# Kernel optimization log

Hardware: AMD Instinct MI355X
Metric: run time of the kernel (lower is better)

## Reference

```python
import jax, jax.numpy as jnp
import numpy as np

B, S, H = 2, 2048, 2048
NH, NKV, HD = 16, 4, 128
THETA = 10000.0


def _rope_cos_sin(seq_len, head_dim, theta, dtype):
    inv_freq = 1.0 / (theta ** (jnp.arange(0, head_dim, 2, dtype=jnp.float32) / head_dim))
    t = jnp.arange(seq_len, dtype=jnp.float32)
    freqs = t[:, None] * inv_freq[None, :]          # [S, HD/2]
    emb = jnp.concatenate([freqs, freqs], axis=-1)  # [S, HD]
    return jnp.cos(emb).astype(dtype), jnp.sin(emb).astype(dtype)


def _rotate_half(x):
    d = x.shape[-1] // 2
    return jnp.concatenate([-x[..., d:], x[..., :d]], axis=-1)


def setup_inputs() -> dict:
    key = jax.random.key(0)
    ks = jax.random.split(key, 5)
    x = jax.random.normal(ks[0], (B, S, H), dtype=jnp.float32)
    Wq = jax.random.normal(ks[1], (NH * HD, H), dtype=jnp.float32) * 0.02
    Wk = jax.random.normal(ks[2], (NKV * HD, H), dtype=jnp.float32) * 0.02
    Wv = jax.random.normal(ks[3], (NKV * HD, H), dtype=jnp.float32) * 0.02
    Wo = jax.random.normal(ks[4], (H, H), dtype=jnp.float32) * 0.02
    causal = jnp.tril(jnp.ones((S, S), dtype=bool))
    attention_mask = jnp.where(causal, 0.0, -1e9).astype(jnp.float32)[None, None]  # [1,1,S,S]
    return {"x": x, "attention_mask": attention_mask, "Wq": Wq, "Wk": Wk, "Wv": Wv, "Wo": Wo}


def reference(x, attention_mask, Wq, Wk, Wv, Wo):
    b, s, _ = x.shape
    q = (x @ Wq.T).reshape(b, s, NH, HD).transpose(0, 2, 1, 3)    # [b,nh,s,hd]
    k = (x @ Wk.T).reshape(b, s, NKV, HD).transpose(0, 2, 1, 3)   # [b,nkv,s,hd]
    v = (x @ Wv.T).reshape(b, s, NKV, HD).transpose(0, 2, 1, 3)
    cos, sin = _rope_cos_sin(s, HD, THETA, x.dtype)               # [s,hd] each
    cos = cos[None, None]; sin = sin[None, None]
    q = q * cos + _rotate_half(q) * sin
    k = k * cos + _rotate_half(k) * sin
    rep = NH // NKV
    k = jnp.repeat(k, rep, axis=1)                                 # [b,nh,s,hd]
    v = jnp.repeat(v, rep, axis=1)
    scores = jnp.einsum('bhqd,bhkd->bhqk', q, k) / jnp.sqrt(jnp.asarray(HD, x.dtype))
    scores = scores + attention_mask
    attn = jax.nn.softmax(scores, axis=-1)
    out = jnp.einsum('bhqk,bhkd->bhqd', attn, v)                   # [b,nh,s,hd]
    out = out.transpose(0, 2, 1, 3).reshape(b, s, NH * HD)
    return out @ Wo.T
```

## Files before the change

kernel.cpp:

```cpp
#include <hip/hip_runtime.h>

typedef unsigned short u16;
typedef __bf16 bf16x8 __attribute__((ext_vector_type(8)));
typedef float f32x4 __attribute__((ext_vector_type(4)));
typedef short s16x4 __attribute__((ext_vector_type(4)));

#define S_LEN  2048
#define NHEADS 16
#define NKVH   4
#define HDIM   128
#define BB     2
#define MROWS  4096
#define QKV_N  3072
#define HID    2048

__device__ __forceinline__ u16 f2b(float f) {
  union { float f; unsigned u; } x; x.f = f;
  unsigned r = x.u + 0x7fffu + ((x.u >> 16) & 1u);
  return (u16)(r >> 16);
}
__device__ __forceinline__ float b2f(u16 v) {
  union { unsigned u; float f; } x; x.u = ((unsigned)v) << 16;
  return x.f;
}
__device__ __forceinline__ void gload_lds16(const u16* g, u16* l) {
  __builtin_amdgcn_global_load_lds((__attribute__((address_space(1))) void*)g,
                                   (__attribute__((address_space(3))) void*)l,
                                   16, 0, 0);
}
__device__ __forceinline__ unsigned cvtpk(float lo, float hi) {
  unsigned r;
  asm("v_cvt_pk_bf16_f32 %0, %1, %2" : "=v"(r) : "v"(lo), "v"(hi));
  return r;
}
__device__ __forceinline__ float fexp2(float x) {
  float r;
  asm("v_exp_f32 %0, %1" : "=v"(r) : "v"(x));
  return r;
}
#if __has_builtin(__builtin_amdgcn_mfma_f32_16x16x16bf16_1k)
__device__ __forceinline__ f32x4 mfma16(s16x4 a, s16x4 b, f32x4 c) {
  return __builtin_amdgcn_mfma_f32_16x16x16bf16_1k(a, b, c, 0, 0, 0);
}
#else
__device__ __forceinline__ f32x4 mfma16(s16x4 a, s16x4 b, f32x4 c) {
  f32x4 d;
  asm volatile("v_mfma_f32_16x16x16_bf16 %0, %1, %2, %3"
               : "=v"(d) : "v"(a), "v"(b), "v"(c));
  return d;
}
#endif

#define SBAR() do { __builtin_amdgcn_sched_barrier(0); \
                    __builtin_amdgcn_s_barrier();      \
                    __builtin_amdgcn_sched_barrier(0); } while (0)

#define PB_X   8192
#define PB_WQ  (PB_X + 4096)
#define PB_WK  (PB_WQ + 1024)
#define PB_WV  (PB_WK + 1024)
#define PB_WO  (PB_WV + 4096)
#define PB_CS  (PB_WO + 512)
__global__ void k_prep(const float* __restrict__ x,
                       const float* __restrict__ Wq, const float* __restrict__ Wk,
                       const float* __restrict__ Wv, const float* __restrict__ Wo,
                       u16* __restrict__ xb, u16* __restrict__ Wqkvb,
                       u16* __restrict__ Wob, float* __restrict__ cs)
{
  const int bid = blockIdx.x, tid = threadIdx.x;
  const float* src; u16* dst; int i;
  if (bid < PB_X)       { i = bid * 256 + tid;            src = x;  dst = xb; }
  else if (bid < PB_WQ) { i = (bid - PB_X) * 256 + tid;   src = Wq; dst = Wqkvb; }
  else if (bid < PB_WK) { i = (bid - PB_WQ) * 256 + tid;  src = Wk; dst = Wqkvb + (size_t)2048 * HID; }
  else if (bid < PB_WV) { i = (bid - PB_WK) * 256 + tid;  src = Wv; dst = Wqkvb + (size_t)2560 * HID; }
  else if (bid < PB_WO) { i = (bid - PB_WV) * 256 + tid;  src = Wo; dst = Wob; }
  else {
    const int p = (bid - PB_WO) * 256 + tid;
    const int s = p >> 6, j = p & 63;
    float inv = expf(-(float)j * 0.14391156831212787f);
    float ang = (float)s * inv;
    float c, sn; sincosf(ang, &sn, &c);
    cs[p * 2 + 0] = c; cs[p * 2 + 1] = sn;
    return;
  }
  float4 v = ((const float4*)src)[i];
  ushort4 o;
  o.x = f2b(v.x); o.y = f2b(v.y); o.z = f2b(v.z); o.w = f2b(v.w);
  ((ushort4*)dst)[i] = o;
}

#define MFMA_GRP(AV, BV, MO, NO)                                              \
  __builtin_amdgcn_s_setprio(1);                                              \
  _Pragma("unroll") for (int kk = 0; kk < 2; ++kk)                            \
  _Pragma("unroll") for (int mm = 0; mm < 4; ++mm)                            \
  _Pragma("unroll") for (int nn = 0; nn < 2; ++nn)                            \
    acc[(MO) + mm][(NO) + nn] = __builtin_amdgcn_mfma_f32_16x16x32_bf16(      \
        AV[kk][mm], BV[kk][nn], acc[(MO) + mm][(NO) + nn], 0, 0, 0);          \
  __builtin_amdgcn_s_setprio(0);

template <int OUT_BF16>
__global__ __launch_bounds__(512, 2) void k_gemm256(
    const u16* __restrict__ A, const u16* __restrict__ Bm, void* __restrict__ Cv,
    int M, int N, int K)
{
  __shared__ u16 AL[2][2][8192];
  __shared__ u16 BL[2][2][8192];
  const int tid = threadIdx.x;
  const int wave = tid >> 6, lane = tid & 63;
  const int l15 = lane & 15, l4 = lane >> 4;
  const int wr = wave >> 2, wc = wave & 3;
  const int gx = gridDim.x;
  const int nwg = gx * gridDim.y;
  int bid = blockIdx.y * gx + blockIdx.x;
  bid = (bid & 7) * (nwg >> 3) + (bid >> 3);
  const int col0 = (bid % gx) * 256, row0 = (bid / gx) * 256;

  int srcOff[2], dstD[2];
#pragma unroll
  for (int li = 0; li < 2; ++li) {
    const int D = (li * 512 + tid) * 16;
    const int off_p = D & 1023, si = D >> 10;
    const int off_l = off_p ^ (((off_p >> 9) & 1) << 5);
    const int R = si >> 1, C = si & 1;
    const int row = R * 16 + (off_l >> 6);
    const int colb = C * 64 + (off_l & 63);
    srcOff[li] = row * K + (colb >> 1);
    dstD[li] = D;
  }
  const int laneoff = (l15 * 64 + l4 * 16) ^ ((l15 >> 3) << 5);

  auto stage = [&](const u16* __restrict__ G, int grow0, int kb, u16* lds) {
#pragma unroll
    for (int li = 0; li < 2; ++li)
      gload_lds16(G + (size_t)grow0 * K + kb + srcOff[li],
                  (u16*)((char*)lds + dstD[li]));
  };

  f32x4 acc[8][4];
#pragma unroll
  for (int m = 0; m < 8; ++m)
#pragma unroll
    for (int n = 0; n < 4; ++n) acc[m][n] = f32x4{0.f, 0.f, 0.f, 0.f};

  const int nk = K >> 6;
  stage(A,  row0,       0,  &AL[0][0][0]);
  stage(A,  row0 + 128, 0,  &AL[0][1][0]);
  stage(Bm, col0,       0,  &BL[0][0][0]);
  stage(Bm, col0 + 128, 0,  &BL[0][1][0]);
  stage(A,  row0,       64, &AL[1][0][0]);
  stage(A,  row0 + 128, 64, &AL[1][1][0]);
  asm volatile("s_waitcnt vmcnt(4)" ::: "memory");
  SBAR();

  for (int t = 0; t < nk; ++t) {
    const int bi = t & 1;
    const bool sB = (t + 1 < nk);
    const bool sA = (t + 2 < nk);
    const char* Ab = (const char*)&AL[bi][wr][0];
    const char* Bb = (const char*)&BL[bi][wc >> 1][0] + (wc & 1) * 8192;
    bf16x8 a0[2][4], a1[2][4], b0[2][2], b1[2][2];
#pragma unroll
    for (int kk = 0; kk < 2; ++kk)
#pragma unroll
      for (int m = 0; m < 4; ++m)
        a0[kk][m] = *(const bf16x8*)(Ab + m * 2048 + kk * 1024 + laneoff);
#pragma unroll
    for (int kk = 0; kk < 2; ++kk)
#pragma unroll
      for (int n = 0; n < 2; ++n)
        b0[kk][n] = *(const bf16x8*)(Bb + n * 2048 + kk * 1024 + laneoff);
    if (sB) stage(Bm, col0, (t + 1) * 64, &BL[bi ^ 1][0][0]);
    SBAR();
    MFMA_GRP(a0, b0, 0, 0);
    SBAR();
#pragma unroll
    for (int kk = 0; kk < 2; ++kk)
#pragma unroll
      for (int m = 0; m < 4; ++m)
        a1[kk][m] = *(const bf16x8*)(Ab + (m + 4) * 2048 + kk * 1024 + laneoff);
    if (sB) stage(Bm, col0 + 128, (t + 1) * 64, &BL[bi ^ 1][1][0]);
    SBAR();
    MFMA_GRP(a1, b0, 4, 0);
    SBAR();
#pragma unroll
    for (int kk = 0; kk < 2; ++kk)
#pragma unroll
      for (int n = 0; n < 2; ++n)
        b1[kk][n] = *(const bf16x8*)(Bb + (n + 2) * 2048 + kk * 1024 + laneoff);
    if (sA) stage(A, row0, (t + 2) * 64, &AL[bi][0][0]);
    SBAR();
    MFMA_GRP(a1, b1, 4, 2);
    SBAR();
    if (sA) {
      stage(A, row0 + 128, (t + 2) * 64, &AL[bi][1][0]);
      asm volatile("s_waitcnt vmcnt(4)" ::: "memory");
    } else if (sB) {
      asm volatile("s_waitcnt vmcnt(0)" ::: "memory");
    }
    SBAR();
    MFMA_GRP(a0, b1, 0, 2);
    SBAR();
  }

#pragma unroll
  for (int m = 0; m < 8; ++m) {
    const int r = row0 + wr * 128 + m * 16 + l4 * 4;
#pragma unroll
    for (int n = 0; n < 4; ++n) {
      const int c = col0 + wc * 64 + n * 16 + l15;
#pragma unroll
      for (int j = 0; j < 4; ++j) {
        const float v = acc[m][n][j];
        if (OUT_BF16) ((u16*)Cv)[(size_t)(r + j) * N + c] = f2b(v);
        else          ((float*)Cv)[(size_t)(r + j) * N + c] = v;
      }
    }
  }
}

template <int OUT_BF16>
__global__ __launch_bounds__(256) void k_gemm_bt(
    const u16* __restrict__ A, const u16* __restrict__ Bm, void* __restrict__ Cv,
    int M, int N, int K)
{
  __shared__ u16 Al[128 * 32];
  __shared__ u16 Bl[128 * 32];
  const int tid = threadIdx.x;
  const int wave = tid >> 6, lane = tid & 63;
  const int l15 = lane & 15, l4 = lane >> 4;
  const int wr = wave >> 1, wc = wave & 1;
  const int row0 = blockIdx.y * 128, col0 = blockIdx.x * 128;

  f32x4 zero = {0.f, 0.f, 0.f, 0.f};
  f32x4 acc[4][4];
#pragma unroll
  for (int m = 0; m < 4; ++m)
#pragma unroll
    for (int n = 0; n < 4; ++n) acc[m][n] = zero;

  const int e0 = lane * 8;
  for (int kb = 0; kb < K; kb += 32) {
#pragma unroll
    for (int it = 0; it < 2; ++it) {
      const int chunk = it * 4 + wave;
      const int e = chunk * 512 + e0;
      const int r = e >> 5, c = e & 31;
      gload_lds16(A + (size_t)(row0 + r) * K + kb + c, Al + chunk * 512);
      gload_lds16(Bm + (size_t)(col0 + r) * K + kb + c, Bl + chunk * 512);
    }
    __syncthreads();
    bf16x8 af[4], bfv[4];
#pragma unroll
    for (int m = 0; m < 4; ++m)
      af[m] = *(const bf16x8*)(Al + (wr * 64 + m * 16 + l15) * 32 + l4 * 8);
#pragma unroll
    for (int n = 0; n < 4; ++n)
      bfv[n] = *(const bf16x8*)(Bl + (wc * 64 + n * 16 + l15) * 32 + l4 * 8);
#pragma unroll
    for (int m = 0; m < 4; ++m)
#pragma unroll
      for (int n = 0; n < 4; ++n)
        acc[m][n] = __builtin_amdgcn_mfma_f32_16x16x32_bf16(af[m], bfv[n], acc[m][n], 0, 0, 0);
    __syncthreads();
  }
#pragma unroll
  for (int m = 0; m < 4; ++m) {
    const int r = row0 + wr * 64 + m * 16 + l4 * 4;
#pragma unroll
    for (int n = 0; n < 4; ++n) {
      const int c = col0 + wc * 64 + n * 16 + l15;
#pragma unroll
      for (int j = 0; j < 4; ++j) {
        const float v = acc[m][n][j];
        if (OUT_BF16) ((u16*)Cv)[(size_t)(r + j) * N + c] = f2b(v);
        else          ((float*)Cv)[(size_t)(r + j) * N + c] = v;
      }
    }
  }
}

__global__ __launch_bounds__(256) void k_ropev(
    const u16* __restrict__ qkv, const float* __restrict__ cs,
    u16* __restrict__ Qr, u16* __restrict__ Kr, u16* __restrict__ Vt)
{
  const int blk = blockIdx.x;
  const int b = blk >> 8, s0 = (blk & 255) << 3;
  const int tid = threadIdx.x;
  const float S2 = 0.08838834764831845f * 1.4426950408889634f;
#pragma unroll
  for (int p = tid; p < 8192; p += 256) {
    const int s = p >> 10, rem = p & 1023, h = rem >> 6, j = rem & 63;
    const int sg = s0 + s;
    const float c = cs[(sg * 64 + j) * 2], sn = cs[(sg * 64 + j) * 2 + 1];
    const u16* src = qkv + (size_t)(b * S_LEN + sg) * QKV_N + h * 128;
    const float x0 = b2f(src[j]), x1 = b2f(src[64 + j]);
    const size_t base = ((size_t)(b * NHEADS + h) * S_LEN + sg) * HDIM;
    Qr[base + j]      = f2b((x0 * c - x1 * sn) * S2);
    Qr[base + 64 + j] = f2b((x1 * c + x0 * sn) * S2);
  }
#pragma unroll
  for (int p = tid; p < 2048; p += 256) {
    const int s = p >> 8, rem = p & 255, h = rem >> 6, j = rem & 63;
    const int sg = s0 + s;
    const float c = cs[(sg * 64 + j) * 2], sn = cs[(sg * 64 + j) * 2 + 1];
    const u16* src = qkv + (size_t)(b * S_LEN + sg) * QKV_N + 2048 + h * 128;
    const float x0 = b2f(src[j]), x1 = b2f(src[64 + j]);
    const size_t base = ((size_t)(b * NKVH + h) * S_LEN + sg) * HDIM;
    Kr[base + j]      = f2b(x0 * c - x1 * sn);
    Kr[base + 64 + j] = f2b(x1 * c + x0 * sn);
  }
#pragma unroll
  for (int vi = 0; vi < 2; ++vi) {
    const int idx = vi * 256 + tid, h = idx >> 7, d = idx & 127;
    union { u16 u[8]; uint4 v; } bb;
#pragma unroll
    for (int s = 0; s < 8; ++s)
      bb.u[s] = qkv[(size_t)(b * S_LEN + s0 + s) * QKV_N + 2560 + idx];
    *(uint4*)(Vt + ((size_t)(b * NKVH + h) * HDIM + d) * S_LEN + s0) = bb.v;
  }
}

__global__ __launch_bounds__(256) void k_attn(
    const u16* __restrict__ Q, const u16* __restrict__ Kr,
    const u16* __restrict__ Vt, u16* __restrict__ Out)
{
  __shared__ u16 Kl[2][64 * 128];
  __shared__ u16 Vl[2][128 * 64];
  const int tid = threadIdx.x;
  const int wave = tid >> 6, lane = tid & 63;
  const int l15 = lane & 15, l4 = lane >> 4;
  const int bid = blockIdx.x;
  const int xg = bid & 7;
  const int b = xg >> 2, kvh = xg & 3;
  const int h = kvh * 4 + ((bid >> 3) & 3);
  const int qt = 15 - (bid >> 5);

  const u16* Kg = Kr + (size_t)(b * NKVH + kvh) * S_LEN * HDIM;
  const u16* Vg = Vt + (size_t)(b * NKVH + kvh) * HDIM * S_LEN;

  int ko[4], vo[4];
#pragma unroll
  for (int it = 0; it < 4; ++it) {
    const int c = it * 4 + wave;
    const int L = c * 1024 + lane * 16;
    const int r = L >> 8;  const int w2 = (L & 255) ^ ((r & 7) << 4);
    ko[it] = r * HDIM + (w2 >> 1);
    const int d = L >> 7;  const int wv = (L & 127) ^ ((d & 7) << 4);
    vo[it] = d * S_LEN + (wv >> 1);
  }

  const int qw0 = qt * 128 + wave * 32;
  const u16* Qg = Q + ((size_t)(b * NHEADS + h) * S_LEN + qw0) * HDIM;

  bf16x8 qf[2][4];
#pragma unroll
  for (int mq = 0; mq < 2; ++mq)
#pragma unroll
    for (int kc = 0; kc < 4; ++kc)
      qf[mq][kc] = *(const bf16x8*)(Qg + (mq * 16 + l15) * HDIM + kc * 32 + l4 * 8);

  f32x4 zero = {0.f, 0.f, 0.f, 0.f};
  f32x4 oacc[2][8];
#pragma unroll
  for (int mq = 0; mq < 2; ++mq)
#pragma unroll
    for (int i = 0; i < 8; ++i) oacc[mq][i] = zero;
  float m_r[2] = {-1e30f, -1e30f}, l_p[2] = {0.f, 0.f};

  const int nt = 2 * qt + 2;
  const int qgl = qw0 + l15;
  int cur = 0;

#pragma unroll
  for (int it = 0; it < 4; ++it)
    gload_lds16(Kg + ko[it], &Kl[0][(it * 4 + wave) * 512]);
#pragma unroll
  for (int it = 0; it < 4; ++it)
    gload_lds16(Vg + (size_t)vo[it], &Vl[0][(it * 4 + wave) * 512]);

  for (int t = 0; t < nt; ++t) {
    const int kt = t * 64;
    asm volatile("s_waitcnt vmcnt(4)" ::: "memory");
    SBAR();
    const char* Kb = (const char*)(cur ? &Kl[1][0] : &Kl[0][0]);
    const char* Vb = (const char*)(cur ? &Vl[1][0] : &Vl[0][0]);
    f32x4 s[2][4];
#pragma unroll
    for (int mq = 0; mq < 2; ++mq)
#pragma unroll
      for (int n = 0; n < 4; ++n) s[mq][n] = zero;
    __builtin_amdgcn_s_setprio(1);
#pragma unroll
    for (int n = 0; n < 4; ++n) {
      const int row = n * 16 + l15;
#pragma unroll
      for (int kc = 0; kc < 4; ++kc) {
        const int ab = (row * 256 + kc * 64 + l4 * 16) ^ ((row & 7) << 4);
        bf16x8 kf = *(const bf16x8*)(Kb + ab);
        s[0][n] = __builtin_amdgcn_mfma_f32_16x16x32_bf16(kf, qf[0][kc], s[0][n], 0, 0, 0);
        s[1][n] = __builtin_amdgcn_mfma_f32_16x16x32_bf16(kf, qf[1][kc], s[1][n], 0, 0, 0);
      }
    }
    __builtin_amdgcn_s_setprio(0);
    const int hasNext = (t + 1 < nt);
    if (hasNext) {
      const int ktn = kt + 64;
      u16* Kn = cur ? &Kl[0][0] : &Kl[1][0];
      u16* Vn = cur ? &Vl[0][0] : &Vl[1][0];
#pragma unroll
      for (int it = 0; it < 4; ++it)
        gload_lds16(Kg + (size_t)ktn * HDIM + ko[it], Kn + (it * 4 + wave) * 512);
#pragma unroll
      for (int it = 0; it < 4; ++it)
        gload_lds16(Vg + (size_t)vo[it] + ktn, Vn + (it * 4 + wave) * 512);
    }
    float sv[2][4][4];
    if (kt + 63 > qw0) {
#pragma unroll
      for (int mq = 0; mq < 2; ++mq)
#pragma unroll
        for (int n = 0; n < 4; ++n)
#pragma unroll
          for (int j = 0; j < 4; ++j) {
            float x = s[mq][n][j];
            if (kt + n * 16 + l4 * 4 + j > qgl + mq * 16) x = -1e30f;
            sv[mq][n][j] = x;
          }
    } else {
#pragma unroll
      for (int mq = 0; mq < 2; ++mq)
#pragma unroll
        for (int n = 0; n < 4; ++n)
#pragma unroll
          for (int j = 0; j < 4; ++j) sv[mq][n][j] = s[mq][n][j];
    }
    float pm[2];
#pragma unroll
    for (int mq = 0; mq < 2; ++mq) {
      pm[mq] = sv[mq][0][0];
#pragma unroll
      for (int n = 0; n < 4; ++n)
#pragma unroll
        for (int j = 0; j < 4; ++j) pm[mq] = fmaxf(pm[mq], sv[mq][n][j]);
    }
    const bool ok = (pm[0] <= m_r[0] + 11.5416f) && (pm[1] <= m_r[1] + 11.5416f);
    if (!__all(ok)) {
#pragma unroll
      for (int mq = 0; mq < 2; ++mq) {
        float pf = fmaxf(pm[mq], __shfl_xor(pm[mq], 16, 64));
        pf = fmaxf(pf, __shfl_xor(pf, 32, 64));
        const float mn = fmaxf(m_r[mq], pf);
        const float sc = fexp2(m_r[mq] - mn);
        m_r[mq] = mn;
        l_p[mq] *= sc;
        float scq[4];
#pragma unroll
        for (int j = 0; j < 4; ++j) scq[j] = __shfl(sc, l4 * 4 + j, 64);
#pragma unroll
        for (int nd = 0; nd < 8; ++nd)
#pragma unroll
          for (int j = 0; j < 4; ++j) oacc[mq][nd][j] *= scq[j];
      }
    }
    union { unsigned u[2]; s16x4 v; } a[2][4];
#pragma unroll
    for (int mq = 0; mq < 2; ++mq)
#pragma unroll
      for (int n = 0; n < 4; ++n) {
        const float p0 = fexp2(sv[mq][n][0] - m_r[mq]);
        const float p1 = fexp2(sv[mq][n][1] - m_r[mq]);
        const float p2 = fexp2(sv[mq][n][2] - m_r[mq]);
        const float p3 = fexp2(sv[mq][n][3] - m_r[mq]);
        l_p[mq] += (p0 + p1) + (p2 + p3);
        a[mq][n].u[0] = cvtpk(p0, p1);
        a[mq][n].u[1] = cvtpk(p2, p3);
      }
    if (hasNext) asm volatile("s_waitcnt vmcnt(8)" ::: "memory");
    else         asm volatile("s_waitcnt vmcnt(0)" ::: "memory");
    SBAR();
    __builtin_amdgcn_s_setprio(1);
#pragma unroll
    for (int nd = 0; nd < 8; ++nd) {
      const int d = nd * 16 + l15;
      const int rowb = d * 128, swz = (d & 7) << 4;
#pragma unroll
      for (int n = 0; n < 4; ++n) {
        const int ab = (rowb + n * 32 + l4 * 8) ^ swz;
        s16x4 vf = *(const s16x4*)(Vb + ab);
        oacc[0][nd] = mfma16(a[0][n].v, vf, oacc[0][nd]);
        oacc[1][nd] = mfma16(a[1][n].v, vf, oacc[1][nd]);
      }
    }
    __builtin_amdgcn_s_setprio(0);
    cur ^= 1;
  }

#pragma unroll
  for (int mq = 0; mq < 2; ++mq) {
    float lp = l_p[mq];
    lp += __shfl_xor(lp, 16, 64);
    lp += __shfl_xor(lp, 32, 64);
    float il[4];
#pragma unroll
    for (int j = 0; j < 4; ++j) il[j] = 1.f / __shfl(lp, l4 * 4 + j, 64);
    const size_t obase =
        ((size_t)b * S_LEN + qw0 + mq * 16 + l4 * 4) * HID + h * HDIM;
#pragma unroll
    for (int nd = 0; nd < 8; ++nd)
#pragma unroll
      for (int j = 0; j < 4; ++j)
        Out[obase + (size_t)j * HID + nd * 16 + l15] = f2b(oacc[mq][nd][j] * il[j]);
  }
}

extern "C" void kernel_launch(void* const* d_in, const int* in_sizes, int n_in,
                              void* d_out, int out_size, void* d_ws, size_t ws_size,
                              hipStream_t stream)
{
  const float* x  = (const float*)d_in[0];
  const float* Wq = (const float*)d_in[2];
  const float* Wk = (const float*)d_in[3];
  const float* Wv = (const float*)d_in[4];
  const float* Wo = (const float*)d_in[5];
  float* out = (float*)d_out;

  u16* xb    = (u16*)d_ws;
  u16* Wqkvb = xb    + (size_t)MROWS * HID;
  u16* Wob   = Wqkvb + (size_t)QKV_N * HID;
  u16* qkv   = Wob   + (size_t)HID * HID;
  u16* Qr    = qkv   + (size_t)MROWS * QKV_N;
  u16* Kr    = Qr    + (size_t)BB * NHEADS * S_LEN * HDIM;
  u16* Vt    = Kr    + (size_t)BB * NKVH * S_LEN * HDIM;
  u16* attn  = Vt    + (size_t)BB * NKVH * S_LEN * HDIM;
  float* cs  = (float*)(attn + (size_t)MROWS * HID);

  k_prep<<<dim3(PB_CS), 256, 0, stream>>>(x, Wq, Wk, Wv, Wo, xb, Wqkvb, Wob, cs);
  k_gemm256<1><<<dim3(QKV_N / 256, MROWS / 256), 512, 0, stream>>>(xb, Wqkvb, qkv, MROWS, QKV_N, HID);
  k_ropev<<<dim3(BB * 256), 256, 0, stream>>>(qkv, cs, Qr, Kr, Vt);
  k_attn<<<dim3(512), 256, 0, stream>>>(Qr, Kr, Vt, attn);
  k_gemm_bt<0><<<dim3(HID / 128, MROWS / 128), 256, 0, stream>>>(attn, Wob, out, MROWS, HID, HID);
}
```

Baseline: 234.3 us.

## Double-buffer GEMM LDS tiles and rebalance attention causal tile ordering

The BT GEMM now uses two LDS buffers, so the next K slice is prefetched while MFMAs run on the current one, with raised wave priority around the MFMA block. This is meant to hide global-load latency behind compute, at the cost of doubled shared memory, which may lower occupancy. The attention kernel changes its query-tile mapping: the first 256 blocks go in ascending order and the rest in descending order, to balance causal work across dispatch waves. It also masks scores in place instead of copying them into a separate array.

```diff
diff --git a/kernel.cpp b/kernel.cpp
--- a/kernel.cpp
+++ b/kernel.cpp
@@ -223,8 +223,8 @@
     const u16* __restrict__ A, const u16* __restrict__ Bm, void* __restrict__ Cv,
     int M, int N, int K)
 {
-  __shared__ u16 Al[128 * 32];
-  __shared__ u16 Bl[128 * 32];
+  __shared__ u16 Al[2][128 * 32];
+  __shared__ u16 Bl[2][128 * 32];
   const int tid = threadIdx.x;
   const int wave = tid >> 6, lane = tid & 63;
   const int l15 = lane & 15, l4 = lane >> 4;
@@ -239,29 +239,40 @@
     for (int n = 0; n < 4; ++n) acc[m][n] = zero;
 
   const int e0 = lane * 8;
-  for (int kb = 0; kb < K; kb += 32) {
+  auto stage = [&](int buf, int kb) {
 #pragma unroll
     for (int it = 0; it < 2; ++it) {
       const int chunk = it * 4 + wave;
       const int e = chunk * 512 + e0;
       const int r = e >> 5, c = e & 31;
-      gload_lds16(A + (size_t)(row0 + r) * K + kb + c, Al + chunk * 512);
-      gload_lds16(Bm + (size_t)(col0 + r) * K + kb + c, Bl + chunk * 512);
-    }
-    __syncthreads();
+      gload_lds16(A + (size_t)(row0 + r) * K + kb + c, &Al[buf][chunk * 512]);
+      gload_lds16(Bm + (size_t)(col0 + r) * K + kb + c, &Bl[buf][chunk * 512]);
+    }
+  };
+
+  stage(0, 0);
+  asm volatile("s_waitcnt vmcnt(0)" ::: "memory");
+  SBAR();
+  int cur = 0;
+  for (int kb = 0; kb < K; kb += 32) {
+    if (kb + 32 < K) stage(cur ^ 1, kb + 32);
     bf16x8 af[4], bfv[4];
 #pragma unroll
     for (int m = 0; m < 4; ++m)
-      af[m] = *(const bf16x8*)(Al + (wr * 64 + m * 16 + l15) * 32 + l4 * 8);
+      af[m] = *(const bf16x8*)(&Al[cur][(wr * 64 + m * 16 + l15) * 32 + l4 * 8]);
 #pragma unroll
     for (int n = 0; n < 4; ++n)
-      bfv[n] = *(const bf16x8*)(Bl + (wc * 64 + n * 16 + l15) * 32 + l4 * 8);
+      bfv[n] = *(const bf16x8*)(&Bl[cur][(wc * 64 + n * 16 + l15) * 32 + l4 * 8]);
+    __builtin_amdgcn_s_setprio(1);
 #pragma unroll
     for (int m = 0; m < 4; ++m)
 #pragma unroll
       for (int n = 0; n < 4; ++n)
         acc[m][n] = __builtin_amdgcn_mfma_f32_16x16x32_bf16(af[m], bfv[n], acc[m][n], 0, 0, 0);
-    __syncthreads();
+    __builtin_amdgcn_s_setprio(0);
+    asm volatile("s_waitcnt vmcnt(0)" ::: "memory");
+    SBAR();
+    cur ^= 1;
   }
 #pragma unroll
   for (int m = 0; m < 4; ++m) {
@@ -333,7 +344,8 @@
   const int xg = bid & 7;
   const int b = xg >> 2, kvh = xg & 3;
   const int h = kvh * 4 + ((bid >> 3) & 3);
-  const int qt = 15 - (bid >> 5);
+  const int qti = bid >> 5;
+  const int qt = (bid < 256) ? qti : 23 - qti;
 
   const u16* Kg = Kr + (size_t)(b * NKVH + kvh) * S_LEN * HDIM;
   const u16* Vg = Vt + (size_t)(b * NKVH + kvh) * HDIM * S_LEN;
@@ -414,34 +426,23 @@
       for (int it = 0; it < 4; ++it)
         gload_lds16(Vg + (size_t)vo[it] + ktn, Vn + (it * 4 + wave) * 512);
     }
-    float sv[2][4][4];
     if (kt + 63 > qw0) {
 #pragma unroll
       for (int mq = 0; mq < 2; ++mq)
 #pragma unroll
         for (int n = 0; n < 4; ++n)
 #pragma unroll
-          for (int j = 0; j < 4; ++j) {
-            float x = s[mq][n][j];
-            if (kt + n * 16 + l4 * 4 + j > qgl + mq * 16) x = -1e30f;
-            sv[mq][n][j] = x;
-          }
-    } else {
-#pragma unroll
-      for (int mq = 0; mq < 2; ++mq)
-#pragma unroll
-        for (int n = 0; n < 4; ++n)
-#pragma unroll
-          for (int j = 0; j < 4; ++j) sv[mq][n][j] = s[mq][n][j];
+          for (int j = 0; j < 4; ++j)
+            if (kt + n * 16 + l4 * 4 + j > qgl + mq * 16) s[mq][n][j] = -1e30f;
     }
     float pm[2];
 #pragma unroll
     for (int mq = 0; mq < 2; ++mq) {
-      pm[mq] = sv[mq][0][0];
+      pm[mq] = s[mq][0][0];
 #pragma unroll
       for (int n = 0; n < 4; ++n)
 #pragma unroll
-        for (int j = 0; j < 4; ++j) pm[mq] = fmaxf(pm[mq], sv[mq][n][j]);
+        for (int j = 0; j < 4; ++j) pm[mq] = fmaxf(pm[mq], s[mq][n][j]);
     }
     const bool ok = (pm[0] <= m_r[0] + 11.5416f) && (pm[1] <= m_r[1] + 11.5416f);
     if (!__all(ok)) {
@@ -467,10 +468,10 @@
     for (int mq = 0; mq < 2; ++mq)
 #pragma unroll
       for (int n = 0; n < 4; ++n) {
-        const float p0 = fexp2(sv[mq][n][0] - m_r[mq]);
-        const float p1 = fexp2(sv[mq][n][1] - m_r[mq]);
-        const float p2 = fexp2(sv[mq][n][2] - m_r[mq]);
-        const float p3 = fexp2(sv[mq][n][3] - m_r[mq]);
+        const float p0 = fexp2(s[mq][n][0] - m_r[mq]);
+        const float p1 = fexp2(s[mq][n][1] - m_r[mq]);
+        const float p2 = fexp2(s[mq][n][2] - m_r[mq]);
+        const float p3 = fexp2(s[mq][n][3] - m_r[mq]);
         l_p[mq] += (p0 + p1) + (p2 + p3);
         a[mq][n].u[0] = cvtpk(p0, p1);
         a[mq][n].u[1] = cvtpk(p2, p3);
```

After: 225.5 us. 3.7% less time.
